# Optimization experiments

Measured on AMD Instinct MI355X. Metric: run time of the kernel, lower is better.

The kernel has to match this reference:

```python
import jax, jax.numpy as jnp
import numpy as np
from jax import lax

K_ADA = 0.1
EPS = 1e-5
B, G = 2, 96
C0, C1, C2, C3, F = 1, 16, 32, 64, 64


def adanorm(x, g):
    # AdaNorm over the last (channel) axis: w * (1 - k*xn) * xn
    mean = x.mean(-1, keepdims=True)
    var = ((x - mean) ** 2).mean(-1, keepdims=True) + EPS
    xn = (x - mean) * lax.rsqrt(var)
    return g * (1.0 - K_ADA * xn) * xn


def conv3d(x, w, b, stride):
    # x: [B,D,H,W,Cin], w: [3,3,3,Cin,Cout], padding 1
    y = lax.conv_general_dilated(x, w, (stride,) * 3, [(1, 1)] * 3,
                                 dimension_numbers=('NDHWC', 'DHWIO', 'NDHWC'))
    return y + b


def downsample_mask(m):
    # active output sites of SparseConv3d(k=3, s=2, p=1): any active input in window
    return lax.reduce_window(m, 0.0, lax.max, (1, 3, 3, 3), (1, 2, 2, 2),
                             [(0, 0), (1, 1), (1, 1), (1, 1)])


def setup_inputs() -> dict:
    key = jax.random.key(0)
    ks = jax.random.split(key, 20)
    mask = (jax.random.uniform(ks[0], (B, G, G, G)) < 0.05).astype(jnp.float32)
    x = jax.random.normal(ks[1], (B, G, G, G, C0), jnp.float32) * mask[..., None]

    def wconv(k, cin, cout):
        return jax.random.normal(k, (3, 3, 3, cin, cout), jnp.float32) / np.sqrt(27.0 * cin)

    inp = {'x': x, 'mask': mask}
    chans = [(C0, C1), (C1, C2), (C2, C2), (C2, C3), (C3, C3)]
    for i, (ci, co) in enumerate(chans, start=1):
        inp[f'w{i}'] = wconv(ks[2 * i], ci, co)
        inp[f'b{i}'] = jax.random.normal(ks[2 * i + 1], (co,), jnp.float32) * 0.01
        inp[f'g{i}'] = jnp.ones((co,), jnp.float32)
    inp['wh'] = jax.random.normal(ks[12], (C3, F), jnp.float32) / np.sqrt(C3)
    inp['bh'] = jax.random.normal(ks[13], (F,), jnp.float32) * 0.01
    inp['gh'] = jnp.ones((F,), jnp.float32)
    return inp


def reference(x, mask, w1, b1, g1, w2, b2, g2, w3, b3, g3, w4, b4, g4, w5, b5, g5, wh, bh, gh):
    m1 = mask
    h = conv3d(x, w1, b1, 1) * m1[..., None]            # SubMConv3d
    h = jax.nn.relu(adanorm(h, g1)) * m1[..., None]
    m2 = downsample_mask(m1)
    h = conv3d(h, w2, b2, 2) * m2[..., None]            # SparseConv3d s=2
    h = jax.nn.relu(adanorm(h, g2)) * m2[..., None]
    h = conv3d(h, w3, b3, 1) * m2[..., None]            # SubMConv3d
    h = jax.nn.relu(adanorm(h, g3)) * m2[..., None]
    m3 = downsample_mask(m2)
    h = conv3d(h, w4, b4, 2) * m3[..., None]            # SparseConv3d s=2
    h = jax.nn.relu(adanorm(h, g4)) * m3[..., None]
    h = conv3d(h, w5, b5, 1) * m3[..., None]            # SubMConv3d
    h = jax.nn.relu(adanorm(h, g5)) * m3[..., None]
    # SparseGlobalMaxPool over active voxels
    neg = jnp.asarray(-3.0e38, h.dtype)
    pooled = jnp.where(m3[..., None] > 0, h, neg).max(axis=(1, 2, 3))  # [B, C3]
    # head: Linear -> AdaNorm -> ReLU -> Dropout(eval = identity)
    out = jax.nn.relu(adanorm(pooled @ wh + bh, gh))
    return out
```

## Files before the change

### kernel.cpp

```cpp
#include <hip/hip_runtime.h>
#include <math.h>

#define K_ADA 0.1f
#define NEPS 1e-5f

typedef __attribute__((ext_vector_type(8))) short short8;
typedef __attribute__((ext_vector_type(4))) float f32x4;
typedef unsigned short ushort_t;

__device__ __forceinline__ ushort_t f2b(float f) {
    union { float f; unsigned u; } v; v.f = f;
    unsigned r = (v.u + 0x7fffu + ((v.u >> 16) & 1u)) >> 16;
    return (ushort_t)r;
}

__device__ __forceinline__ float wave_sum64(float v) {
#pragma unroll
    for (int m = 1; m < 64; m <<= 1) v += __shfl_xor(v, m, 64);
    return v;
}

__host__ __device__ constexpr int tapd2(int tap) {
    return tap >= 27 ? 0 : (tap / 9) * 81 + ((tap / 3) % 3) * 9 + (tap % 3);
}

template <int CIN, int COUT>
__device__ __forceinline__ void pack_w_el(const float* __restrict__ w,
                                          ushort_t* __restrict__ wp, int t)
{
    constexpr int NKH = CIN / 32;
    constexpr int NCT = COUT / 16;
    int jj = t & 7;
    int lane = (t >> 3) & 63;
    int rest = t >> 9;
    int kh = rest % NKH;
    int rest2 = rest / NKH;
    int ct = rest2 % NCT;
    int tap = rest2 / NCT;
    int cin = kh * 32 + (lane >> 4) * 8 + jj;
    int cout = ct * 16 + (lane & 15);
    wp[t] = f2b(w[(tap * CIN + cin) * COUT + cout]);
}

__global__ __launch_bounds__(256) void prep_k(
    const float* __restrict__ w1, const float* __restrict__ w2,
    const float* __restrict__ w3, const float* __restrict__ w4,
    const float* __restrict__ w5, const float* __restrict__ m1,
    ushort_t* __restrict__ wp1, ushort_t* __restrict__ wp2,
    ushort_t* __restrict__ wp3, ushort_t* __restrict__ wp4,
    ushort_t* __restrict__ wp5, float* __restrict__ m2,
    float* __restrict__ zeropad, int* __restrict__ counters,
    float* __restrict__ pooled)
{
    int t = blockIdx.x * 256 + threadIdx.x;
    if (t < 512) {
        int jj = t & 7;
        int lane = t >> 3;
        int tap = (lane >> 4) * 8 + jj;
        int cout = lane & 15;
        wp1[t] = (tap < 27) ? f2b(w1[tap * 16 + cout]) : (ushort_t)0;
    } else if (t < 14848) {
        int u = t - 512;
        int jj = u & 7;
        int lane = (u >> 3) & 63;
        int rest = u >> 9;
        int ct = rest & 1;
        int p = rest >> 1;
        int tap = 2 * p + (lane >> 5);
        int cin = ((lane >> 4) & 1) * 8 + jj;
        int cout = ct * 16 + (lane & 15);
        wp2[u] = (tap < 27) ? f2b(w2[(tap * 16 + cin) * 32 + cout]) : (ushort_t)0;
    } else if (t < 42496) {
        pack_w_el<32, 32>(w3, wp3, t - 14848);
    } else if (t < 97792) {
        pack_w_el<32, 64>(w4, wp4, t - 42496);
    } else if (t < 208384) {
        pack_w_el<64, 64>(w5, wp5, t - 97792);
    } else if (t < 429568) {
        int v = t - 208384;
        constexpr int GO = 48, GI = 96;
        int b = v / (GO * GO * GO);
        int r = v % (GO * GO * GO);
        int d = r / (GO * GO), h = (r / GO) % GO, x = r % GO;
        float mx = 0.f;
        for (int kd = 0; kd < 3; ++kd) {
            int zd = 2 * d + kd - 1; if ((unsigned)zd >= GI) continue;
            for (int kh = 0; kh < 3; ++kh) {
                int zh = 2 * h + kh - 1; if ((unsigned)zh >= GI) continue;
                for (int kw = 0; kw < 3; ++kw) {
                    int zx = 2 * x + kw - 1; if ((unsigned)zx >= GI) continue;
                    mx = fmaxf(mx, m1[((b * GI + zd) * GI + zh) * GI + zx]);
                }
            }
        }
        m2[v] = mx;
    } else if (t < 429576) {
        zeropad[t - 429568] = 0.f;
    } else if (t < 431624) {
        counters[t - 429576] = 0;
    } else if (t < 431752) {
        pooled[t - 431624] = 0.f;
    }
}

template <int GO, int GI>
__global__ __launch_bounds__(256) void dmask_k(const float* __restrict__ mi,
                                               float* __restrict__ mo)
{
    constexpr int N = 2 * GO * GO * GO;
    int v = blockIdx.x * 256 + threadIdx.x;
    if (v >= N) return;
    int b = v / (GO * GO * GO);
    int r = v % (GO * GO * GO);
    int d = r / (GO * GO), h = (r / GO) % GO, x = r % GO;
    float mx = 0.f;
    for (int kd = 0; kd < 3; ++kd) {
        int zd = 2 * d + kd - 1; if ((unsigned)zd >= GI) continue;
        for (int kh = 0; kh < 3; ++kh) {
            int zh = 2 * h + kh - 1; if ((unsigned)zh >= GI) continue;
            for (int kw = 0; kw < 3; ++kw) {
                int zx = 2 * x + kw - 1; if ((unsigned)zx >= GI) continue;
                mx = fmaxf(mx, mi[((b * GI + zd) * GI + zh) * GI + zx]);
            }
        }
    }
    mo[v] = mx;
}

__global__ __launch_bounds__(256) void conv1_fill_k(const float* __restrict__ m1,
                                                    int* __restrict__ list,
                                                    int* __restrict__ counters)
{
    int v = blockIdx.x * 256 + threadIdx.x;
    bool act = (m1[v] != 0.f);
    unsigned long long msk = __ballot(act);
    int lane = threadIdx.x & 63;
    int gwave = v >> 6;
    int p = gwave & 63;
    int base = 0;
    int cnt = __popcll(msk);
    if (lane == 0 && cnt) base = atomicAdd(&counters[p * 32], cnt);
    base = __shfl(base, 0, 64);
    if (act) {
        int pre = __popcll(msk & ((1ull << lane) - 1ull));
        list[p * 27648 + base + pre] = v;
    }
}

__global__ __launch_bounds__(256) void conv1_act_k(const float* __restrict__ x,
                                                   const int* __restrict__ list,
                                                   const int* __restrict__ counters,
                                                   const ushort_t* __restrict__ wp1,
                                                   const float* __restrict__ bias,
                                                   const float* __restrict__ gain,
                                                   const float* __restrict__ zerof,
                                                   ushort_t* __restrict__ h1b)
{
    constexpr int G = 96, G3 = G * G * G;
    int gwave = (blockIdx.x * 256 + threadIdx.x) >> 6;
    int p = gwave & 63;
    int lw = gwave >> 6;
    int nact = counters[p * 32];
    if (nact <= 0) return;
    const int* plist = list + p * 27648;
    int lane = threadIdx.x & 63;
    int m = lane & 15, q = lane >> 4;
    int nchunk = (nact + 15) >> 4;
    float bn = bias[m], gn = gain[m];
    short8 bfr = *reinterpret_cast<const short8*>(wp1 + lane * 8);

    for (int chunk = lw; chunk < nchunk; chunk += 54) {
        int idx = chunk * 16 + m;
        int vm = plist[min(idx, nact - 1)];
        int b = vm / G3;
        int rr = vm % G3;
        int dm = rr / (G * G), hm = (rr / G) % G, xm = rr % G;

        float xs[8];
#pragma unroll
        for (int j = 0; j < 8; ++j) {
            int k = q * 8 + j;
            int kd = k / 9, kh = (k / 3) % 3, kw = k % 3;
            int id = dm + kd - 1, ih = hm + kh - 1, ix = xm + kw - 1;
            bool ok = (k < 27) && ((unsigned)id < (unsigned)G) &&
                      ((unsigned)ih < (unsigned)G) && ((unsigned)ix < (unsigned)G);
            const float* xp = ok ? (x + (((size_t)b * G + id) * G + ih) * G + ix) : zerof;
            xs[j] = *xp;
        }
        ushort_t av[8];
#pragma unroll
        for (int j = 0; j < 8; ++j) av[j] = f2b(xs[j]);
        short8 a = *reinterpret_cast<short8*>(av);
        f32x4 acc = {0.f, 0.f, 0.f, 0.f};
        acc = __builtin_amdgcn_mfma_f32_16x16x32_bf16(a, bfr, acc, 0, 0, 0);

#pragma unroll
        for (int i = 0; i < 4; ++i) {
            int oidx = chunk * 16 + q * 4 + i;
            float xv = acc[i] + bn;
            float s = xv;
#pragma unroll
            for (int mk = 1; mk < 16; mk <<= 1) s += __shfl_xor(s, mk, 64);
            float mean = s * (1.f / 16.f);
            float dd = xv - mean;
            float ss = dd * dd;
#pragma unroll
            for (int mk = 1; mk < 16; mk <<= 1) ss += __shfl_xor(ss, mk, 64);
            float rs = rsqrtf(ss * (1.f / 16.f) + NEPS);
            float xn = dd * rs;
            float o = fmaxf(gn * (1.f - K_ADA * xn) * xn, 0.f);
            if (oidx < nact) {
                int w = plist[oidx];
                h1b[(size_t)w * 16 + m] = f2b(o);
            }
        }
    }
}

__global__ __launch_bounds__(256, 4) void conv2_tile_k(
    const ushort_t* __restrict__ h1b, const float* __restrict__ m1,
    const ushort_t* __restrict__ wp2,
    const float* __restrict__ bias, const float* __restrict__ gain,
    const float* __restrict__ m2, const float* __restrict__ zerof,
    ushort_t* __restrict__ h2b)
{
    constexpr int GI = 96, G = 48;
    __shared__ __align__(16) ushort_t halo[729 * 3 * 8];

    int bid = blockIdx.x;
    int b = bid / 1728;
    int r = bid % 1728;
    int td = r / 144, th = (r / 12) % 12, tx = r % 12;
    int d0 = 4 * td, h0 = 4 * th, x0 = 4 * tx;
    int bd = 2 * d0 - 1, bh = 2 * h0 - 1, bx = 2 * x0 - 1;

    const ushort_t* zp = (const ushort_t*)zerof;
    for (int c = threadIdx.x; c < 1458; c += 256) {
        int hv = c >> 1, j = c & 1;
        int gd = bd + hv / 81;
        int gh = bh + (hv / 9) % 9;
        int gx = bx + hv % 9;
        bool inb = ((unsigned)gd < (unsigned)GI) && ((unsigned)gh < (unsigned)GI) &&
                   ((unsigned)gx < (unsigned)GI);
        size_t gi = (((size_t)b * GI + gd) * GI + gh) * GI + gx;
        const float* mp = inb ? (m1 + gi) : zerof;
        float mv = *mp;
        const ushort_t* p = (mv != 0.f) ? (h1b + gi * 16 + j * 8) : zp;
        *reinterpret_cast<short8*>(halo + ((size_t)hv * 3 + j) * 8) =
            *reinterpret_cast<const short8*>(p);
    }
    __syncthreads();

    int wv = threadIdx.x >> 6;
    int lane = threadIdx.x & 63;
    int m = lane & 15, q = lane >> 4;
    int mh = m >> 2, mx = m & 3;
    int tq = q >> 1, hq = q & 1;
    int hbase = 162 * wv + 18 * mh + 2 * mx;

    f32x4 acc0 = {0.f, 0.f, 0.f, 0.f}, acc1 = acc0;
#pragma unroll
    for (int g = 0; g < 2; ++g) {
        short8 a[7], b0[7], b1[7];
#pragma unroll
        for (int j = 0; j < 7; ++j) {
            const int p = g * 7 + j;
            int hv = hbase + (tq ? tapd2(2 * p + 1) : tapd2(2 * p));
            a[j] = *reinterpret_cast<const short8*>(halo + ((size_t)hv * 3 + hq) * 8);
            b0[j] = *reinterpret_cast<const short8*>(wp2 + ((size_t)(p * 2 + 0) * 64 + lane) * 8);
            b1[j] = *reinterpret_cast<const short8*>(wp2 + ((size_t)(p * 2 + 1) * 64 + lane) * 8);
        }
#pragma unroll
        for (int j = 0; j < 7; ++j) {
            acc0 = __builtin_amdgcn_mfma_f32_16x16x32_bf16(a[j], b0[j], acc0, 0, 0, 0);
            acc1 = __builtin_amdgcn_mfma_f32_16x16x32_bf16(a[j], b1[j], acc1, 0, 0, 0);
        }
    }

    float b0s = bias[m], b1s = bias[16 + m];
    float g0s = gain[m], g1s = gain[16 + m];
#pragma unroll
    for (int i = 0; i < 4; ++i) {
        int rr2 = q * 4 + i;
        int w = ((b * G + d0 + wv) * G + h0 + (rr2 >> 2)) * G + x0 + (rr2 & 3);
        float xv0 = acc0[i] + b0s;
        float xv1 = acc1[i] + b1s;
        float s = xv0 + xv1;
#pragma unroll
        for (int mk = 1; mk < 16; mk <<= 1) s += __shfl_xor(s, mk, 64);
        float mean = s * (1.f / 32.f);
        float dd0 = xv0 - mean, dd1 = xv1 - mean;
        float ss = dd0 * dd0 + dd1 * dd1;
#pragma unroll
        for (int mk = 1; mk < 16; mk <<= 1) ss += __shfl_xor(ss, mk, 64);
        float rs = rsqrtf(ss * (1.f / 32.f) + NEPS);
        float mv = m2[w];
        float xn0 = dd0 * rs, xn1 = dd1 * rs;
        float o0 = fmaxf(g0s * (1.f - K_ADA * xn0) * xn0, 0.f);
        float o1 = fmaxf(g1s * (1.f - K_ADA * xn1) * xn1, 0.f);
        if (mv == 0.f) { o0 = 0.f; o1 = 0.f; }
        h2b[(size_t)w * 32 + m]      = f2b(o0);
        h2b[(size_t)w * 32 + 16 + m] = f2b(o1);
    }
}

__global__ __launch_bounds__(256, 3) void conv3_tile_k(
    const ushort_t* __restrict__ h2b, const ushort_t* __restrict__ wp3,
    const float* __restrict__ bias, const float* __restrict__ gain,
    const float* __restrict__ m2, const ushort_t* __restrict__ zp,
    ushort_t* __restrict__ h3b)
{
    constexpr int G = 48;
    __shared__ __align__(16) ushort_t halo[216 * 5 * 8];
    __shared__ float nbuf[64][33];

    int bid = blockIdx.x;
    int b = bid / 1728;
    int r = bid % 1728;
    int td = r / 144, th = (r / 12) % 12, tx = r % 12;
    int d0 = 4 * td, h0 = 4 * th, x0 = 4 * tx;
    int bd = d0 - 1, bh = h0 - 1, bx = x0 - 1;

    for (int c = threadIdx.x; c < 864; c += 256) {
        int hv = c >> 2, j = c & 3;
        int gd = bd + hv / 36;
        int gh = bh + (hv / 6) % 6;
        int gx = bx + hv % 6;
        bool ok = ((unsigned)gd < (unsigned)G) && ((unsigned)gh < (unsigned)G) &&
                  ((unsigned)gx < (unsigned)G);
        const ushort_t* p = ok ? (h2b + ((((size_t)b * G + gd) * G + gh) * G + gx) * 32 + j * 8) : zp;
        *reinterpret_cast<short8*>(halo + ((size_t)hv * 5 + j) * 8) =
            *reinterpret_cast<const short8*>(p);
    }
    __syncthreads();

    int wv = threadIdx.x >> 6;
    int lane = threadIdx.x & 63;
    int m = lane & 15, q = lane >> 4;
    int mh = m >> 2, mx = m & 3;
    int ct = wv & 1;
    int sp = wv >> 1;
    int hb0 = 36 * (2 * sp) + 6 * mh + mx;
    int hb1 = hb0 + 36;

    f32x4 acc0 = {0.f, 0.f, 0.f, 0.f}, acc1 = acc0;
#pragma unroll
    for (int g = 0; g < 3; ++g) {
        short8 a0[9], a1[9], bb[9];
#pragma unroll
        for (int j = 0; j < 9; ++j) {
            const int tap = g * 9 + j;
            const int dlt = (tap / 9) * 36 + ((tap / 3) % 3) * 6 + (tap % 3);
            a0[j] = *reinterpret_cast<const short8*>(halo + ((size_t)(hb0 + dlt) * 5 + q) * 8);
            a1[j] = *reinterpret_cast<const short8*>(halo + ((size_t)(hb1 + dlt) * 5 + q) * 8);
            bb[j] = *reinterpret_cast<const short8*>(
                wp3 + ((size_t)(tap * 2 + ct) * 64 + lane) * 8);
        }
#pragma unroll
        for (int j = 0; j < 9; ++j) {
            acc0 = __builtin_amdgcn_mfma_f32_16x16x32_bf16(a0[j], bb[j], acc0, 0, 0, 0);
            acc1 = __builtin_amdgcn_mfma_f32_16x16x32_bf16(a1[j], bb[j], acc1, 0, 0, 0);
        }
    }

    float bn = bias[ct * 16 + m];
#pragma unroll
    for (int i = 0; i < 4; ++i) {
        int rr2 = q * 4 + i;
        nbuf[(2 * sp) * 16 + rr2][ct * 16 + m]     = acc0[i] + bn;
        nbuf[(2 * sp + 1) * 16 + rr2][ct * 16 + m] = acc1[i] + bn;
    }
    __syncthreads();

    int hh = lane >> 5;
    int ch = lane & 31;
    float gns = gain[ch];
#pragma unroll
    for (int it = 0; it < 8; ++it) {
        int vloc = wv * 16 + it * 2 + hh;
        float val = nbuf[vloc][ch];
        float s = val;
#pragma unroll
        for (int mk = 1; mk < 32; mk <<= 1) s += __shfl_xor(s, mk, 64);
        float mean = s * (1.f / 32.f);
        float dd = val - mean;
        float ss = dd * dd;
#pragma unroll
        for (int mk = 1; mk < 32; mk <<= 1) ss += __shfl_xor(ss, mk, 64);
        float rs = rsqrtf(ss * (1.f / 32.f) + NEPS);
        int slice = vloc >> 4, rr2 = vloc & 15;
        int w = ((b * G + d0 + slice) * G + h0 + (rr2 >> 2)) * G + x0 + (rr2 & 3);
        float xn = dd * rs;
        float o = fmaxf(gns * (1.f - K_ADA * xn) * xn, 0.f);
        if (m2[w] == 0.f) o = 0.f;
        h3b[(size_t)w * 32 + ch] = f2b(o);
    }
}

template <int G_IN, int CIN, int STRIDE, bool POOL>
__global__ __launch_bounds__(256, 4) void conv45_tile_k(
    const ushort_t* __restrict__ Ab, const ushort_t* __restrict__ Wp,
    const float* __restrict__ bias, const float* __restrict__ gain,
    const float* __restrict__ mask,
    ushort_t* __restrict__ outb, unsigned* __restrict__ pooled)
{
    constexpr int G = 24;
    constexpr int NKH = CIN / 32;
    constexpr int NCH = CIN / 8;
    constexpr int PADC = NCH + 1;
    constexpr int HD = STRIDE + 3;
    constexpr int HH = STRIDE + 3;
    constexpr int HX = 3 * STRIDE + 3;
    constexpr int NHV = HD * HH * HX;
    constexpr int NCHUNK = NHV * NCH;

    __shared__ __align__(16) ushort_t halo[NHV * PADC * 8];
    __shared__ float nbuf[16][65];
    __shared__ float pbuf[4][64];

    int bid = blockIdx.x;
    int b = bid / 864;
    int r = bid % 864;
    int td = r / 72, th = (r / 6) % 12, tx = r % 6;
    int d0 = 2 * td, h0 = 2 * th, x0 = 4 * tx;
    int bd = d0 * STRIDE - 1, bh = h0 * STRIDE - 1, bx = x0 * STRIDE - 1;

    for (int c = threadIdx.x; c < NCHUNK; c += 256) {
        int hv = c / NCH, j = c % NCH;
        int gd = bd + hv / (HH * HX);
        int gh = bh + (hv / HX) % HH;
        int gx = bx + hv % HX;
        short8 val = {0, 0, 0, 0, 0, 0, 0, 0};
        if ((unsigned)gd < (unsigned)G_IN && (unsigned)gh < (unsigned)G_IN &&
            (unsigned)gx < (unsigned)G_IN)
            val = *reinterpret_cast<const short8*>(
                Ab + ((((size_t)b * G_IN + gd) * G_IN + gh) * G_IN + gx) * CIN + j * 8);
        *reinterpret_cast<short8*>(halo + ((size_t)hv * PADC + j) * 8) = val;
    }
    __syncthreads();

    int ct = threadIdx.x >> 6;
    int lane = threadIdx.x & 63;
    int m = lane & 15, q = lane >> 4;
    int md = (m >> 3) & 1, mh = (m >> 2) & 1, mx = m & 3;

    f32x4 acc = {0.f, 0.f, 0.f, 0.f};
    constexpr int NT = 27 * NKH;
    constexpr int GSZ = 9;
#pragma unroll
    for (int g = 0; g < NT / GSZ; ++g) {
        short8 ab[GSZ], bb[GSZ];
#pragma unroll
        for (int j = 0; j < GSZ; ++j) {
            int it = g * GSZ + j;
            int tap = it / NKH, k2 = it % NKH;
            const int kd = tap / 9, kh = (tap / 3) % 3, kw = tap % 3;
            int hv = ((md * STRIDE + kd) * HH + (mh * STRIDE + kh)) * HX +
                     (mx * STRIDE + kw);
            ab[j] = *reinterpret_cast<const short8*>(
                halo + ((size_t)hv * PADC + k2 * 4 + q) * 8);
            bb[j] = *reinterpret_cast<const short8*>(
                Wp + (((size_t)(tap * 4 + ct) * NKH + k2) * 64 + lane) * 8);
        }
#pragma unroll
        for (int j = 0; j < GSZ; ++j)
            acc = __builtin_amdgcn_mfma_f32_16x16x32_bf16(ab[j], bb[j], acc, 0, 0, 0);
    }

    float bn = bias[ct * 16 + m];
#pragma unroll
    for (int i = 0; i < 4; ++i) nbuf[q * 4 + i][ct * 16 + m] = acc[i] + bn;
    __syncthreads();

    float gn = gain[lane];
    float wavemax = 0.f;
#pragma unroll
    for (int i = 0; i < 4; ++i) {
        int vloc = ct * 4 + i;
        int vd = d0 + ((vloc >> 3) & 1);
        int vh = h0 + ((vloc >> 2) & 1);
        int vx = x0 + (vloc & 3);
        int w = ((b * G + vd) * G + vh) * G + vx;
        float val = nbuf[vloc][lane];
        float mean = wave_sum64(val) * (1.f / 64.f);
        float dd = val - mean;
        float var = wave_sum64(dd * dd) * (1.f / 64.f) + NEPS;
        float xn = dd * rsqrtf(var);
        float o = fmaxf(gn * (1.f - K_ADA * xn) * xn, 0.f);
        if (mask[w] == 0.f) o = 0.f;
        if (POOL) wavemax = fmaxf(wavemax, o);
        else      outb[(size_t)w * 64 + lane] = f2b(o);
    }
    if (POOL) {
        pbuf[ct][lane] = wavemax;
        __syncthreads();
        if (ct == 0) {
            float v = fmaxf(fmaxf(pbuf[0][lane], pbuf[1][lane]),
                            fmaxf(pbuf[2][lane], pbuf[3][lane]));
            atomicMax(&pooled[b * 64 + lane], __float_as_uint(v));
        }
    }
}

__global__ __launch_bounds__(128) void head_k(const float* __restrict__ pooled,
                                              const float* __restrict__ wh,
                                              const float* __restrict__ bh,
                                              const float* __restrict__ gh,
                                              float* __restrict__ out)
{
    __shared__ float pl[2][64];
    int t = threadIdx.x;
    int b = t >> 6;
    int f = t & 63;
    pl[b][f] = pooled[b * 64 + f];
    __syncthreads();
    float acc = bh[f];
#pragma unroll
    for (int k = 0; k < 64; ++k) acc += pl[b][k] * wh[k * 64 + f];
    float mean = wave_sum64(acc) * (1.f / 64.f);
    float dd = acc - mean;
    float var = wave_sum64(dd * dd) * (1.f / 64.f) + NEPS;
    float xn = dd * rsqrtf(var);
    float val = gh[f] * (1.f - K_ADA * xn) * xn;
    out[t] = fmaxf(val, 0.f);
}

extern "C" void kernel_launch(void* const* d_in, const int* in_sizes, int n_in,
                              void* d_out, int out_size, void* d_ws, size_t ws_size,
                              hipStream_t stream)
{
    const float* x  = (const float*)d_in[0];
    const float* m1 = (const float*)d_in[1];
    const float* w1 = (const float*)d_in[2];
    const float* b1 = (const float*)d_in[3];
    const float* g1 = (const float*)d_in[4];
    const float* w2 = (const float*)d_in[5];
    const float* b2 = (const float*)d_in[6];
    const float* g2 = (const float*)d_in[7];
    const float* w3 = (const float*)d_in[8];
    const float* b3 = (const float*)d_in[9];
    const float* g3 = (const float*)d_in[10];
    const float* w4 = (const float*)d_in[11];
    const float* b4 = (const float*)d_in[12];
    const float* g4 = (const float*)d_in[13];
    const float* w5 = (const float*)d_in[14];
    const float* b5 = (const float*)d_in[15];
    const float* g5 = (const float*)d_in[16];
    const float* wh = (const float*)d_in[17];
    const float* bh = (const float*)d_in[18];
    const float* gh = (const float*)d_in[19];
    float* out = (float*)d_out;

    float* ws = (float*)d_ws;
    ushort_t* h1b = (ushort_t*)ws;
    ushort_t* h2b = (ushort_t*)(ws + 14155776);
    ushort_t* h3b = (ushort_t*)(ws + 17694720);
    ushort_t* h4b = (ushort_t*)(ws + 21233664);
    float* m2 = ws + 22118400;
    float* m3 = ws + 22339584;
    ushort_t* wp1 = (ushort_t*)(ws + 22367232);
    ushort_t* wp2 = (ushort_t*)(ws + 22367488);
    ushort_t* wp3 = (ushort_t*)(ws + 22374656);
    ushort_t* wp4 = (ushort_t*)(ws + 22388480);
    ushort_t* wp5 = (ushort_t*)(ws + 22416128);
    float* zeropad = ws + 22471424;
    int* counters = (int*)(ws + 22471432);
    float* pooled = ws + 22473480;
    int* list = (int*)(ws + 14155776);

    prep_k<<<1687, 256, 0, stream>>>(w1, w2, w3, w4, w5, m1,
                                     wp1, wp2, wp3, wp4, wp5, m2, zeropad,
                                     counters, pooled);
    dmask_k<24, 48><<<108, 256, 0, stream>>>(m2, m3);

    const ushort_t* zp = (const ushort_t*)zeropad;
    conv1_fill_k<<<6912, 256, 0, stream>>>(m1, list, counters);
    conv1_act_k<<<864, 256, 0, stream>>>(x, list, counters, wp1, b1, g1, zeropad, h1b);
    conv2_tile_k<<<3456, 256, 0, stream>>>(h1b, m1, wp2, b2, g2, m2, zeropad, h2b);
    conv3_tile_k<<<3456, 256, 0, stream>>>(h2b, wp3, b3, g3, m2, zp, h3b);
    conv45_tile_k<48, 32, 2, false><<<1728, 256, 0, stream>>>(h3b, wp4, b4, g4, m3, h4b, nullptr);
    conv45_tile_k<24, 64, 1, true><<<1728, 256, 0, stream>>>(h4b, wp5, b5, g5, m3, nullptr,
                                                             (unsigned*)pooled);
    head_k<<<1, 128, 0, stream>>>(pooled, wh, bh, gh, out);
}
```

Baseline: 241.2 us.

## Widen conv3 tiles, stage conv2 mask in LDS, fold dmask into fill

The second-level mask downsample now runs as extra blocks of the conv1 fill kernel, which removes one kernel launch. conv2 loads its 9x9x9 m1 mask halo into shared memory once, so the two channel-half loads no longer each re-read the mask from global memory. conv3 tiles grow from 4x4x4 to 4x4x8 voxels, so each weight fragment feeds four MFMA tiles instead of two and the halo overlap per voxel shrinks. In exchange, conv3 uses more LDS and registers per block and launches half as many blocks, which may lower occupancy.

```diff
diff --git a/kernel.cpp b/kernel.cpp
--- a/kernel.cpp
+++ b/kernel.cpp
@@ -103,34 +103,32 @@
     }
 }
 
-template <int GO, int GI>
-__global__ __launch_bounds__(256) void dmask_k(const float* __restrict__ mi,
-                                               float* __restrict__ mo)
-{
-    constexpr int N = 2 * GO * GO * GO;
-    int v = blockIdx.x * 256 + threadIdx.x;
-    if (v >= N) return;
-    int b = v / (GO * GO * GO);
-    int r = v % (GO * GO * GO);
-    int d = r / (GO * GO), h = (r / GO) % GO, x = r % GO;
-    float mx = 0.f;
-    for (int kd = 0; kd < 3; ++kd) {
-        int zd = 2 * d + kd - 1; if ((unsigned)zd >= GI) continue;
-        for (int kh = 0; kh < 3; ++kh) {
-            int zh = 2 * h + kh - 1; if ((unsigned)zh >= GI) continue;
-            for (int kw = 0; kw < 3; ++kw) {
-                int zx = 2 * x + kw - 1; if ((unsigned)zx >= GI) continue;
-                mx = fmaxf(mx, mi[((b * GI + zd) * GI + zh) * GI + zx]);
-            }
-        }
-    }
-    mo[v] = mx;
-}
-
 __global__ __launch_bounds__(256) void conv1_fill_k(const float* __restrict__ m1,
+                                                    const float* __restrict__ m2,
+                                                    float* __restrict__ m3,
                                                     int* __restrict__ list,
                                                     int* __restrict__ counters)
 {
+    if (blockIdx.x >= 6912) {
+        int v = (blockIdx.x - 6912) * 256 + threadIdx.x;
+        constexpr int GO = 24, GI = 48;
+        int b = v / (GO * GO * GO);
+        int r = v % (GO * GO * GO);
+        int d = r / (GO * GO), h = (r / GO) % GO, x = r % GO;
+        float mx = 0.f;
+        for (int kd = 0; kd < 3; ++kd) {
+            int zd = 2 * d + kd - 1; if ((unsigned)zd >= GI) continue;
+            for (int kh = 0; kh < 3; ++kh) {
+                int zh = 2 * h + kh - 1; if ((unsigned)zh >= GI) continue;
+                for (int kw = 0; kw < 3; ++kw) {
+                    int zx = 2 * x + kw - 1; if ((unsigned)zx >= GI) continue;
+                    mx = fmaxf(mx, m2[((b * GI + zd) * GI + zh) * GI + zx]);
+                }
+            }
+        }
+        m3[v] = mx;
+        return;
+    }
     int v = blockIdx.x * 256 + threadIdx.x;
     bool act = (m1[v] != 0.f);
     unsigned long long msk = __ballot(act);
@@ -226,6 +224,7 @@
 {
     constexpr int GI = 96, G = 48;
     __shared__ __align__(16) ushort_t halo[729 * 3 * 8];
+    __shared__ float m1h[729];
 
     int bid = blockIdx.x;
     int b = bid / 1728;
@@ -234,18 +233,25 @@
     int d0 = 4 * td, h0 = 4 * th, x0 = 4 * tx;
     int bd = 2 * d0 - 1, bh = 2 * h0 - 1, bx = 2 * x0 - 1;
 
+    for (int c = threadIdx.x; c < 729; c += 256) {
+        int gd = bd + c / 81;
+        int gh = bh + (c / 9) % 9;
+        int gx = bx + c % 9;
+        bool inb = ((unsigned)gd < (unsigned)GI) && ((unsigned)gh < (unsigned)GI) &&
+                   ((unsigned)gx < (unsigned)GI);
+        const float* mp = inb ? (m1 + (((size_t)b * GI + gd) * GI + gh) * GI + gx) : zerof;
+        m1h[c] = *mp;
+    }
+    __syncthreads();
+
     const ushort_t* zp = (const ushort_t*)zerof;
     for (int c = threadIdx.x; c < 1458; c += 256) {
         int hv = c >> 1, j = c & 1;
         int gd = bd + hv / 81;
         int gh = bh + (hv / 9) % 9;
         int gx = bx + hv % 9;
-        bool inb = ((unsigned)gd < (unsigned)GI) && ((unsigned)gh < (unsigned)GI) &&
-                   ((unsigned)gx < (unsigned)GI);
         size_t gi = (((size_t)b * GI + gd) * GI + gh) * GI + gx;
-        const float* mp = inb ? (m1 + gi) : zerof;
-        float mv = *mp;
-        const ushort_t* p = (mv != 0.f) ? (h1b + gi * 16 + j * 8) : zp;
+        const ushort_t* p = (m1h[hv] != 0.f) ? (h1b + gi * 16 + j * 8) : zp;
         *reinterpret_cast<short8*>(halo + ((size_t)hv * 3 + j) * 8) =
             *reinterpret_cast<const short8*>(p);
     }
@@ -311,21 +317,21 @@
     ushort_t* __restrict__ h3b)
 {
     constexpr int G = 48;
-    __shared__ __align__(16) ushort_t halo[216 * 5 * 8];
-    __shared__ float nbuf[64][33];
+    __shared__ __align__(16) ushort_t halo[360 * 5 * 8];
+    __shared__ float nbuf[128][33];
 
     int bid = blockIdx.x;
-    int b = bid / 1728;
-    int r = bid % 1728;
-    int td = r / 144, th = (r / 12) % 12, tx = r % 12;
-    int d0 = 4 * td, h0 = 4 * th, x0 = 4 * tx;
+    int b = bid / 864;
+    int r = bid % 864;
+    int td = r / 72, th = (r / 6) % 12, tx2 = r % 6;
+    int d0 = 4 * td, h0 = 4 * th, x0 = 8 * tx2;
     int bd = d0 - 1, bh = h0 - 1, bx = x0 - 1;
 
-    for (int c = threadIdx.x; c < 864; c += 256) {
+    for (int c = threadIdx.x; c < 1440; c += 256) {
         int hv = c >> 2, j = c & 3;
-        int gd = bd + hv / 36;
-        int gh = bh + (hv / 6) % 6;
-        int gx = bx + hv % 6;
+        int gd = bd + hv / 60;
+        int gh = bh + (hv / 10) % 6;
+        int gx = bx + hv % 10;
         bool ok = ((unsigned)gd < (unsigned)G) && ((unsigned)gh < (unsigned)G) &&
                   ((unsigned)gx < (unsigned)G);
         const ushort_t* p = ok ? (h2b + ((((size_t)b * G + gd) * G + gh) * G + gx) * 32 + j * 8) : zp;
@@ -337,38 +343,57 @@
     int wv = threadIdx.x >> 6;
     int lane = threadIdx.x & 63;
     int m = lane & 15, q = lane >> 4;
-    int mh = m >> 2, mx = m & 3;
+    int hloc = m >> 2, xl = m & 3;
     int ct = wv & 1;
-    int sp = wv >> 1;
-    int hb0 = 36 * (2 * sp) + 6 * mh + mx;
-    int hb1 = hb0 + 36;
-
-    f32x4 acc0 = {0.f, 0.f, 0.f, 0.f}, acc1 = acc0;
+    int g2 = wv >> 1;
+    int hb[4];
+#pragma unroll
+    for (int mt = 0; mt < 4; ++mt) {
+        int dsl = 2 * g2 + (mt >> 1);
+        int xh = mt & 1;
+        hb[mt] = dsl * 60 + hloc * 10 + xh * 4 + xl;
+    }
+
+    f32x4 accs[4];
+#pragma unroll
+    for (int mt = 0; mt < 4; ++mt) accs[mt] = {0.f, 0.f, 0.f, 0.f};
+
 #pragma unroll
     for (int g = 0; g < 3; ++g) {
-        short8 a0[9], a1[9], bb[9];
+        short8 bb[9];
 #pragma unroll
         for (int j = 0; j < 9; ++j) {
             const int tap = g * 9 + j;
-            const int dlt = (tap / 9) * 36 + ((tap / 3) % 3) * 6 + (tap % 3);
-            a0[j] = *reinterpret_cast<const short8*>(halo + ((size_t)(hb0 + dlt) * 5 + q) * 8);
-            a1[j] = *reinterpret_cast<const short8*>(halo + ((size_t)(hb1 + dlt) * 5 + q) * 8);
             bb[j] = *reinterpret_cast<const short8*>(
                 wp3 + ((size_t)(tap * 2 + ct) * 64 + lane) * 8);
         }
 #pragma unroll
-        for (int j = 0; j < 9; ++j) {
-            acc0 = __builtin_amdgcn_mfma_f32_16x16x32_bf16(a0[j], bb[j], acc0, 0, 0, 0);
-            acc1 = __builtin_amdgcn_mfma_f32_16x16x32_bf16(a1[j], bb[j], acc1, 0, 0, 0);
+        for (int mt = 0; mt < 4; ++mt) {
+            short8 a[9];
+#pragma unroll
+            for (int j = 0; j < 9; ++j) {
+                const int tap = g * 9 + j;
+                const int dlt = (tap / 9) * 60 + ((tap / 3) % 3) * 10 + (tap % 3);
+                a[j] = *reinterpret_cast<const short8*>(
+                    halo + ((size_t)(hb[mt] + dlt) * 5 + q) * 8);
+            }
+#pragma unroll
+            for (int j = 0; j < 9; ++j)
+                accs[mt] = __builtin_amdgcn_mfma_f32_16x16x32_bf16(a[j], bb[j], accs[mt], 0, 0, 0);
         }
     }
 
     float bn = bias[ct * 16 + m];
 #pragma unroll
-    for (int i = 0; i < 4; ++i) {
-        int rr2 = q * 4 + i;
-        nbuf[(2 * sp) * 16 + rr2][ct * 16 + m]     = acc0[i] + bn;
-        nbuf[(2 * sp + 1) * 16 + rr2][ct * 16 + m] = acc1[i] + bn;
+    for (int mt = 0; mt < 4; ++mt) {
+        int dsl = 2 * g2 + (mt >> 1);
+        int xh = mt & 1;
+#pragma unroll
+        for (int i = 0; i < 4; ++i) {
+            int vrow = q * 4 + i;
+            int vid = dsl * 32 + (vrow >> 2) * 8 + xh * 4 + (vrow & 3);
+            nbuf[vid][ct * 16 + m] = accs[mt][i] + bn;
+        }
     }
     __syncthreads();
 
@@ -376,9 +401,9 @@
     int ch = lane & 31;
     float gns = gain[ch];
 #pragma unroll
-    for (int it = 0; it < 8; ++it) {
-        int vloc = wv * 16 + it * 2 + hh;
-        float val = nbuf[vloc][ch];
+    for (int it = 0; it < 16; ++it) {
+        int vid = wv * 32 + it * 2 + hh;
+        float val = nbuf[vid][ch];
         float s = val;
 #pragma unroll
         for (int mk = 1; mk < 32; mk <<= 1) s += __shfl_xor(s, mk, 64);
@@ -388,8 +413,8 @@
 #pragma unroll
         for (int mk = 1; mk < 32; mk <<= 1) ss += __shfl_xor(ss, mk, 64);
         float rs = rsqrtf(ss * (1.f / 32.f) + NEPS);
-        int slice = vloc >> 4, rr2 = vloc & 15;
-        int w = ((b * G + d0 + slice) * G + h0 + (rr2 >> 2)) * G + x0 + (rr2 & 3);
+        int dsl = vid >> 5, hl = (vid >> 3) & 3, xll = vid & 7;
+        int w = ((b * G + d0 + dsl) * G + h0 + hl) * G + x0 + xll;
         float xn = dd * rs;
         float o = fmaxf(gns * (1.f - K_ADA * xn) * xn, 0.f);
         if (m2[w] == 0.f) o = 0.f;
@@ -571,13 +596,12 @@
     prep_k<<<1687, 256, 0, stream>>>(w1, w2, w3, w4, w5, m1,
                                      wp1, wp2, wp3, wp4, wp5, m2, zeropad,
                                      counters, pooled);
-    dmask_k<24, 48><<<108, 256, 0, stream>>>(m2, m3);
 
     const ushort_t* zp = (const ushort_t*)zeropad;
-    conv1_fill_k<<<6912, 256, 0, stream>>>(m1, list, counters);
+    conv1_fill_k<<<7020, 256, 0, stream>>>(m1, m2, m3, list, counters);
     conv1_act_k<<<864, 256, 0, stream>>>(x, list, counters, wp1, b1, g1, zeropad, h1b);
     conv2_tile_k<<<3456, 256, 0, stream>>>(h1b, m1, wp2, b2, g2, m2, zeropad, h2b);
-    conv3_tile_k<<<3456, 256, 0, stream>>>(h2b, wp3, b3, g3, m2, zp, h3b);
+    conv3_tile_k<<<1728, 256, 0, stream>>>(h2b, wp3, b3, g3, m2, zp, h3b);
     conv45_tile_k<48, 32, 2, false><<<1728, 256, 0, stream>>>(h3b, wp4, b4, g4, m3, h4b, nullptr);
     conv45_tile_k<24, 64, 1, true><<<1728, 256, 0, stream>>>(h4b, wp5, b5, g5, m3, nullptr,
                                                              (unsigned*)pooled);
```

New measurement: 244.4 us. About the same (+1.3%).
